# Kernel tuning notes

Measured on AMD Instinct MI355X. Metric: run time of the kernel, lower is better.

Reference implementation:

```python
import jax, jax.numpy as jnp
import numpy as np


def setup_inputs() -> dict:
    key = jax.random.key(0)
    ks = jax.random.split(key, 6)
    B_, S, D_in, D_out, R, E = 4, 2048, 2048, 2048, 64, 16
    x = jax.random.normal(ks[0], (B_, S, D_in), dtype=jnp.float32)
    W_base = jax.random.normal(ks[1], (D_out, D_in), dtype=jnp.float32) * (D_in ** -0.5)
    b_base = jax.random.normal(ks[2], (D_out,), dtype=jnp.float32) * 0.02
    # orthogonal rows, as get_orthogonal_matrix(reservoir_size, in_features)
    G = np.asarray(jax.random.normal(ks[3], (D_in, R), dtype=jnp.float32))
    Q, _ = np.linalg.qr(G)  # [D_in, R] orthonormal columns
    A = jnp.asarray(Q.T, dtype=jnp.float32)  # [R, D_in]
    # B initialized to zeros in the module; use small random so delta is nontrivial
    Bmat = jax.random.normal(ks[4], (E, D_out, R), dtype=jnp.float32) * 0.02
    W_router = jax.random.normal(ks[5], (E, D_in), dtype=jnp.float32) * 0.02
    return {"x": x, "W_base": W_base, "b_base": b_base, "A": A, "B": Bmat,
            "W_router": W_router, "top_k": 2}


def reference(x, W_base, b_base, A, B, W_router, top_k):
    E = W_router.shape[0]
    base_output = jnp.einsum('bsi,oi->bso', x, W_base) + b_base          # [B,S,D_out]
    res_hidden = jnp.einsum('bsi,ri->bsr', x, A)                          # [B,S,R]
    router_logits = jnp.einsum('bsi,ei->bse', x, W_router)                # [B,S,E]
    routing_weights = jax.nn.softmax(router_logits, axis=-1)
    if top_k > 0 and top_k < E:
        _, top_idx = jax.lax.top_k(routing_weights, top_k)                # [B,S,k]
        mask = jax.nn.one_hot(top_idx, E, dtype=routing_weights.dtype).sum(axis=-2)
        routing_weights = routing_weights * mask
        routing_weights = routing_weights / (routing_weights.sum(axis=-1, keepdims=True) + 1e-6)
    # contract experts+rank without materializing [B,S,E,D_out]
    h = jnp.einsum('bsr,bse->bser', res_hidden, routing_weights)          # [B,S,E,R] (small)
    delta = jnp.einsum('bser,edr->bsd', h, B)                             # [B,S,D_out]
    return base_output + delta
```

## Files before the change

### kernel.cpp

```cpp
#include <hip/hip_runtime.h>
#include <hip/hip_bf16.h>

#define D_IN  2048
#define D_OUT 2048
#define RNK   64
#define NE    16
#define KTOT  3072
#define NTILE 48

typedef __attribute__((ext_vector_type(8))) short bf16x8;
typedef __attribute__((ext_vector_type(4))) float f32x4;
typedef __attribute__((ext_vector_type(16))) float f32x16;

__device__ __forceinline__ void async_ld16(const void* g, void* l) {
    __builtin_amdgcn_global_load_lds(
        (const __attribute__((address_space(1))) void*)g,
        (__attribute__((address_space(3))) void*)l,
        16, 0, 0);
}

__global__ __launch_bounds__(384) void castwa_kernel(
    const float* __restrict__ Wb, const float* __restrict__ Bm,
    const float* __restrict__ A,
    __hip_bfloat16* __restrict__ Wc, __hip_bfloat16* __restrict__ Ab)
{
    const int c = threadIdx.x * 8;
    const float* src;
    __hip_bfloat16* dst;
    if (blockIdx.x < D_OUT) {
        const int n = blockIdx.x;
        if (c < D_IN) {
            src = Wb + (size_t)n * D_IN + c;
        } else {
            const int j = c - D_IN;
            const int e = j >> 6, r = j & 63;
            src = Bm + ((size_t)e * D_OUT + n) * RNK + r;
        }
        dst = Wc + (size_t)n * KTOT + c;
    } else {
        if (c >= D_IN) return;
        const int r = blockIdx.x - D_OUT;
        src = A + (size_t)r * D_IN + c;
        dst = Ab + (size_t)r * D_IN + c;
    }
    const float4 a = *(const float4*)src;
    const float4 b = *(const float4*)(src + 4);
    const float vv[8] = {a.x, a.y, a.z, a.w, b.x, b.y, b.z, b.w};
    union { bf16x8 v; __hip_bfloat16 h[8]; } u;
#pragma unroll
    for (int q = 0; q < 8; ++q) u.h[q] = __float2bfloat16(vv[q]);
    *(bf16x8*)dst = u.v;
}

__global__ __launch_bounds__(512) void prep2_kernel(
    const float* __restrict__ x, const float* __restrict__ Wr,
    const __hip_bfloat16* __restrict__ Ab,
    const int* __restrict__ topk_p, __hip_bfloat16* __restrict__ Xc)
{
    __shared__ __align__(16) char smem[81920];
    __hip_bfloat16* xb = (__hip_bfloat16*)smem;
    float* stage = (float*)(smem + 65536);
    float* red = (float*)smem;
    float* wf  = (float*)(smem + 65536);

    const int tid = threadIdx.x;
    const int wave = tid >> 6, lane = tid & 63;
    const int qm = lane & 15, quad = lane >> 4;
    const int t0 = blockIdx.x * 16;
    const int tA = t0 + wave * 2;

    float acc[NE][2];
#pragma unroll
    for (int e = 0; e < NE; ++e) { acc[e][0] = 0.f; acc[e][1] = 0.f; }

    const float4* x4 = (const float4*)x;
    float4 xv[2], xn[2];
    xv[0] = x4[(size_t)tA * 512 + lane];
    xv[1] = x4[(size_t)(tA + 1) * 512 + lane];

    for (int c = 0; c < 8; ++c) {
        async_ld16(Wr + (size_t)wave * D_IN + c * 256 + lane * 4,
                   (void*)(stage + wave * 256));
        async_ld16(Wr + (size_t)(wave + 8) * D_IN + c * 256 + lane * 4,
                   (void*)(stage + (wave + 8) * 256));
        if (c < 7) {
            xn[0] = x4[(size_t)tA * 512 + (c + 1) * 64 + lane];
            xn[1] = x4[(size_t)(tA + 1) * 512 + (c + 1) * 64 + lane];
        }
        __syncthreads();

#pragma unroll
        for (int t = 0; t < 2; ++t) {
            const int tl = wave * 2 + t;
            union { short4 v; __hip_bfloat16 h[4]; } u;
            u.h[0] = __float2bfloat16(xv[t].x); u.h[1] = __float2bfloat16(xv[t].y);
            u.h[2] = __float2bfloat16(xv[t].z); u.h[3] = __float2bfloat16(xv[t].w);
            *(short4*)(Xc + (size_t)(t0 + tl) * KTOT + c * 256 + lane * 4) = u.v;
            const int gg = c * 32 + (lane >> 1);
            const int pg = gg ^ (tl & 7);
            *(short4*)((char*)xb + tl * 4096 + pg * 16 + (lane & 1) * 8) = u.v;
        }
        const float4* wr4 = (const float4*)stage;
#pragma unroll
        for (int e = 0; e < NE; ++e) {
            const float4 wv = wr4[e * 64 + lane];
            acc[e][0] += xv[0].x*wv.x + xv[0].y*wv.y + xv[0].z*wv.z + xv[0].w*wv.w;
            acc[e][1] += xv[1].x*wv.x + xv[1].y*wv.y + xv[1].z*wv.z + xv[1].w*wv.w;
        }
        __syncthreads();
        if (c < 7) { xv[0] = xn[0]; xv[1] = xn[1]; }
    }

#pragma unroll
    for (int off = 32; off; off >>= 1)
#pragma unroll
        for (int e = 0; e < NE; ++e) {
            acc[e][0] += __shfl_xor(acc[e][0], off, 64);
            acc[e][1] += __shfl_xor(acc[e][1], off, 64);
        }
    if (lane < 2) {
        const int tt = lane;
        const int k = topk_p[0];
        float m = -1e30f;
#pragma unroll
        for (int e = 0; e < NE; ++e) m = fmaxf(m, acc[e][tt]);
        float w[NE]; float ssum = 0.f;
#pragma unroll
        for (int e = 0; e < NE; ++e) { w[e] = __expf(acc[e][tt] - m); ssum += w[e]; }
        const float inv = 1.f / ssum;
#pragma unroll
        for (int e = 0; e < NE; ++e) w[e] *= inv;
        float* wfout = wf + (size_t)(wave * 2 + tt) * NE;
        if (k > 0 && k < NE) {
            int chosen[NE];
#pragma unroll
            for (int e = 0; e < NE; ++e) chosen[e] = 0;
            float ksum = 0.f;
            for (int it = 0; it < k; ++it) {
                int bi = 0; float bv = -1.f;
                for (int e = 0; e < NE; ++e)
                    if (!chosen[e] && w[e] > bv) { bv = w[e]; bi = e; }
                chosen[bi] = 1; ksum += bv;
            }
            const float rinv = 1.f / (ksum + 1e-6f);
            for (int e = 0; e < NE; ++e) wfout[e] = chosen[e] ? w[e] * rinv : 0.f;
        } else {
            for (int e = 0; e < NE; ++e) wfout[e] = w[e];
        }
    }

    f32x4 racc[4] = {};
    const int kb = wave * 256;
#pragma unroll
    for (int s = 0; s < 4; ++s) {
        const int k0 = kb + s * 64;
        const int gg0 = (k0 >> 3) + quad;
        const bf16x8 a0 = *(const bf16x8*)((char*)xb + qm * 4096 + ((gg0 ^ (qm & 7)) * 16));
        const bf16x8 a1 = *(const bf16x8*)((char*)xb + qm * 4096 + (((gg0 + 4) ^ (qm & 7)) * 16));
        bf16x8 b0[4], b1[4];
#pragma unroll
        for (int nf = 0; nf < 4; ++nf) {
            const __hip_bfloat16* bp = Ab + (size_t)(qm + nf * 16) * D_IN + k0 + quad * 8;
            b0[nf] = *(const bf16x8*)bp;
            b1[nf] = *(const bf16x8*)(bp + 32);
        }
#pragma unroll
        for (int nf = 0; nf < 4; ++nf) {
            racc[nf] = __builtin_amdgcn_mfma_f32_16x16x32_bf16(a0, b0[nf], racc[nf], 0, 0, 0);
            racc[nf] = __builtin_amdgcn_mfma_f32_16x16x32_bf16(a1, b1[nf], racc[nf], 0, 0, 0);
        }
    }
    __syncthreads();

#pragma unroll
    for (int nf = 0; nf < 4; ++nf)
#pragma unroll
        for (int r = 0; r < 4; ++r)
            red[(wave * 16 + quad * 4 + r) * 64 + nf * 16 + qm] = racc[nf][r];
    __syncthreads();

#pragma unroll
    for (int it = 0; it < 4; ++it) {
        const int s = it * 512 + tid;
        const int t = s >> 7;
        const int chunk = s & 127;
        const int e = chunk >> 3, r0 = (chunk & 7) * 8;
        const float wgt = wf[t * 16 + e];
        float4 s0 = {0.f, 0.f, 0.f, 0.f}, s1 = {0.f, 0.f, 0.f, 0.f};
#pragma unroll
        for (int w2 = 0; w2 < 8; ++w2) {
            const float4 p0 = ((const float4*)red)[(w2 * 16 + t) * 16 + (r0 >> 2)];
            const float4 p1 = ((const float4*)red)[(w2 * 16 + t) * 16 + (r0 >> 2) + 1];
            s0.x += p0.x; s0.y += p0.y; s0.z += p0.z; s0.w += p0.w;
            s1.x += p1.x; s1.y += p1.y; s1.z += p1.z; s1.w += p1.w;
        }
        union { bf16x8 v; __hip_bfloat16 h[8]; } u;
        u.h[0] = __float2bfloat16(wgt * s0.x); u.h[1] = __float2bfloat16(wgt * s0.y);
        u.h[2] = __float2bfloat16(wgt * s0.z); u.h[3] = __float2bfloat16(wgt * s0.w);
        u.h[4] = __float2bfloat16(wgt * s1.x); u.h[5] = __float2bfloat16(wgt * s1.y);
        u.h[6] = __float2bfloat16(wgt * s1.z); u.h[7] = __float2bfloat16(wgt * s1.w);
        *(bf16x8*)(Xc + (size_t)(t0 + t) * KTOT + D_IN + chunk * 8) = u.v;
    }
}

#define LDA3(BUF, M, ks) (*(const bf16x8*)(smem + (BUF) + \
    ((((M) >> 1) * 128 + wm2 * 64 + ((M) & 1) * 32 + l31) * 128) + \
    (((((ks) * 2 + lhi) ^ (l31 & 7))) << 4)))
#define LDB3(BUF, N, ks) (*(const bf16x8*)(smem + 65536 + (BUF) + \
    ((wn4 * 64 + (N) * 32 + l31) * 128) + \
    (((((ks) * 2 + lhi) ^ (l31 & 7))) << 4)))

#define GP(BUF, MH, ISSUE, WAIT) do { \
    bf16x8 af[2][4]; \
    if ((MH) == 0) { \
        _Pragma("unroll") for (int n = 0; n < 2; ++n) \
        _Pragma("unroll") for (int ks = 0; ks < 4; ++ks) \
            bfr[n][ks] = LDB3(BUF, n, ks); \
    } \
    _Pragma("unroll") for (int m = 0; m < 2; ++m) \
    _Pragma("unroll") for (int ks = 0; ks < 4; ++ks) \
        af[m][ks] = LDA3(BUF, (MH) * 2 + m, ks); \
    ISSUE; \
    __builtin_amdgcn_s_setprio(1); \
    _Pragma("unroll") for (int ks = 0; ks < 4; ++ks) \
    _Pragma("unroll") for (int m = 0; m < 2; ++m) \
    _Pragma("unroll") for (int n = 0; n < 2; ++n) \
        acc[(MH) * 2 + m][n] = __builtin_amdgcn_mfma_f32_32x32x16_bf16( \
            af[m][ks], bfr[n][ks], acc[(MH) * 2 + m][n], 0, 0, 0); \
    __builtin_amdgcn_s_setprio(0); \
    WAIT; \
    __builtin_amdgcn_sched_barrier(0); \
    __builtin_amdgcn_s_barrier(); \
    __builtin_amdgcn_sched_barrier(0); \
} while (0)

__global__ __launch_bounds__(512, 2) void gemm3_kernel(
    const __hip_bfloat16* __restrict__ Am,
    const __hip_bfloat16* __restrict__ Bm,
    const float* __restrict__ bias,
    float* __restrict__ C)
{
    __shared__ __align__(16) char smem[131072];
    const int tid = threadIdx.x;
    const int w = tid >> 6, lane = tid & 63;
    const int l31 = lane & 31, lhi = lane >> 5;
    const int wm2 = w >> 2, wn4 = w & 3;

    int flat = blockIdx.y * gridDim.x + blockIdx.x;
    flat = (flat & 7) * 32 + (flat >> 3);
    const int bm = flat & 31, bn = flat >> 5;

    const int rb0 = w * 16 + (lane >> 3);
    const int rb1 = rb0 + 8;
    const int gs0 = (lane & 7) ^ (rb0 & 7);
    const int gs1 = (lane & 7) ^ (rb1 & 7);
    const __hip_bfloat16* pA0 = Am + (size_t)(bm * 256 + rb0) * KTOT + gs0 * 8;
    const __hip_bfloat16* pA1 = Am + (size_t)(bm * 256 + rb1) * KTOT + gs1 * 8;
    const __hip_bfloat16* pB0 = Bm + (size_t)(bn * 256 + rb0) * KTOT + gs0 * 8;
    const __hip_bfloat16* pB1 = Bm + (size_t)(bn * 256 + rb1) * KTOT + gs1 * 8;
    const size_t HO = (size_t)128 * KTOT;

    f32x16 acc[4][2] = {};
    bf16x8 bfr[2][4];

    auto stageP1 = [&](int tn) {
        const size_t ko = (size_t)tn * 64;
        char* da = smem + (tn & 1) * 32768 + w * 2048;
        async_ld16(pA0 + ko, da);
        async_ld16(pA1 + ko, da + 1024);
        char* db = smem + 65536 + (tn & 1) * 32768 + w * 2048;
        async_ld16(pB0 + ko, db);
        async_ld16(pB1 + ko, db + 1024);
        async_ld16(pB0 + HO + ko, db + 16384);
        async_ld16(pB1 + HO + ko, db + 16384 + 1024);
    };
    auto stageP2 = [&](int tn) {
        const size_t ko = (size_t)tn * 64;
        char* da = smem + (tn & 1) * 32768 + 16384 + w * 2048;
        async_ld16(pA0 + HO + ko, da);
        async_ld16(pA1 + HO + ko, da + 1024);
    };

    stageP1(0); stageP2(0); stageP1(1);
    asm volatile("s_waitcnt vmcnt(8)" ::: "memory");
    __builtin_amdgcn_sched_barrier(0);
    __builtin_amdgcn_s_barrier();
    __builtin_amdgcn_sched_barrier(0);

    for (int t = 0; t < NTILE - 2; ++t) {
        const int bo = (t & 1) * 32768;
        GP(bo, 0, stageP2(t + 1),
           asm volatile("s_waitcnt vmcnt(8)" ::: "memory"));
        GP(bo, 1, stageP1(t + 2),
           asm volatile("s_waitcnt vmcnt(8)" ::: "memory"));
    }
    {
        const int bo = ((NTILE - 2) & 1) * 32768;
        GP(bo, 0, stageP2(NTILE - 1),
           asm volatile("s_waitcnt vmcnt(8)" ::: "memory"));
        GP(bo, 1, ,
           asm volatile("s_waitcnt vmcnt(2)" ::: "memory"));
    }
    {
        const int bo = ((NTILE - 1) & 1) * 32768;
        GP(bo, 0, ,
           asm volatile("s_waitcnt vmcnt(0)" ::: "memory"));
        GP(bo, 1, , );
    }

#pragma unroll
    for (int n = 0; n < 2; ++n) {
        const int col = bn * 256 + wn4 * 64 + n * 32 + l31;
        const float bbv = bias[col];
#pragma unroll
        for (int m = 0; m < 4; ++m) {
            const size_t rbase = (size_t)bm * 256 + (m >> 1) * 128 + wm2 * 64
                               + (m & 1) * 32 + 4 * lhi;
#pragma unroll
            for (int reg = 0; reg < 16; ++reg) {
                const size_t row = rbase + (reg & 3) + 8 * (reg >> 2);
                C[row * D_OUT + col] = acc[m][n][reg] + bbv;
            }
        }
    }
}

extern "C" void kernel_launch(void* const* d_in, const int* in_sizes, int n_in,
                              void* d_out, int out_size, void* d_ws, size_t ws_size,
                              hipStream_t stream) {
    const float* x    = (const float*)d_in[0];
    const float* Wb   = (const float*)d_in[1];
    const float* bb   = (const float*)d_in[2];
    const float* A    = (const float*)d_in[3];
    const float* Bm   = (const float*)d_in[4];
    const float* Wr   = (const float*)d_in[5];
    const int*   topk = (const int*)d_in[6];
    float* out = (float*)d_out;
    const int T = in_sizes[0] / D_IN;

    __hip_bfloat16* Xc = (__hip_bfloat16*)d_ws;
    __hip_bfloat16* Wc = (__hip_bfloat16*)((char*)d_ws + (size_t)T * KTOT * 2);
    __hip_bfloat16* Ab = (__hip_bfloat16*)d_out;

    castwa_kernel<<<D_OUT + RNK, 384, 0, stream>>>(Wb, Bm, A, Wc, Ab);
    prep2_kernel<<<T / 16, 512, 0, stream>>>(x, Wr, Ab, topk, Xc);
    gemm3_kernel<<<dim3(32, 8), 512, 0, stream>>>(Xc, Wc, bb, out);
}
```

Measured before the change: 265.5 us.

## Double-buffer router weight staging in prep kernel and remap GEMM tiles per XCD

The prep kernel now gives each half-wave one token, processes 128-element chunks over 16 iterations, and double-buffers the router-weight staging in LDS. This replaces two __syncthreads per chunk with a single vmcnt wait plus barrier, so loads overlap with compute and the reduction needs fewer shuffle steps. The GEMM block-to-tile mapping is also changed so each XCD works on an 8x4 patch of output tiles, meant to improve L2 reuse of A and B panels. The costs are more loop iterations, a swizzled LDS layout, and an added barrier before the rank projection.

```diff
diff --git a/kernel.cpp b/kernel.cpp
--- a/kernel.cpp
+++ b/kernel.cpp
@@ -59,78 +59,73 @@
 {
     __shared__ __align__(16) char smem[81920];
     __hip_bfloat16* xb = (__hip_bfloat16*)smem;
-    float* stage = (float*)(smem + 65536);
+    float* stg = (float*)(smem + 65536);
     float* red = (float*)smem;
     float* wf  = (float*)(smem + 65536);
 
     const int tid = threadIdx.x;
     const int wave = tid >> 6, lane = tid & 63;
+    const int l31 = lane & 31, lh = lane >> 5;
     const int qm = lane & 15, quad = lane >> 4;
     const int t0 = blockIdx.x * 16;
-    const int tA = t0 + wave * 2;
-
-    float acc[NE][2];
-#pragma unroll
-    for (int e = 0; e < NE; ++e) { acc[e][0] = 0.f; acc[e][1] = 0.f; }
+    const int tl = wave * 2 + lh;
+    const size_t myt = (size_t)t0 + tl;
+
+    float acc[NE];
+#pragma unroll
+    for (int e = 0; e < NE; ++e) acc[e] = 0.f;
 
     const float4* x4 = (const float4*)x;
-    float4 xv[2], xn[2];
-    xv[0] = x4[(size_t)tA * 512 + lane];
-    xv[1] = x4[(size_t)(tA + 1) * 512 + lane];
-
-    for (int c = 0; c < 8; ++c) {
-        async_ld16(Wr + (size_t)wave * D_IN + c * 256 + lane * 4,
-                   (void*)(stage + wave * 256));
-        async_ld16(Wr + (size_t)(wave + 8) * D_IN + c * 256 + lane * 4,
-                   (void*)(stage + (wave + 8) * 256));
-        if (c < 7) {
-            xn[0] = x4[(size_t)tA * 512 + (c + 1) * 64 + lane];
-            xn[1] = x4[(size_t)(tA + 1) * 512 + (c + 1) * 64 + lane];
-        }
-        __syncthreads();
-
-#pragma unroll
-        for (int t = 0; t < 2; ++t) {
-            const int tl = wave * 2 + t;
-            union { short4 v; __hip_bfloat16 h[4]; } u;
-            u.h[0] = __float2bfloat16(xv[t].x); u.h[1] = __float2bfloat16(xv[t].y);
-            u.h[2] = __float2bfloat16(xv[t].z); u.h[3] = __float2bfloat16(xv[t].w);
-            *(short4*)(Xc + (size_t)(t0 + tl) * KTOT + c * 256 + lane * 4) = u.v;
-            const int gg = c * 32 + (lane >> 1);
-            const int pg = gg ^ (tl & 7);
-            *(short4*)((char*)xb + tl * 4096 + pg * 16 + (lane & 1) * 8) = u.v;
-        }
-        const float4* wr4 = (const float4*)stage;
+    const int sg = l31 ^ ((l31 >> 3) & 7);
+    const float* wr_src = Wr + (size_t)tl * D_IN + sg * 4;
+
+    async_ld16(wr_src, (void*)(stg + wave * 256));
+    float4 xv = x4[myt * 512 + l31];
+    float4 xn;
+
+    for (int c = 0; c < 16; ++c) {
+        asm volatile("s_waitcnt vmcnt(1)" ::: "memory");
+        __builtin_amdgcn_sched_barrier(0);
+        __builtin_amdgcn_s_barrier();
+        __builtin_amdgcn_sched_barrier(0);
+        if (c < 15) {
+            async_ld16(wr_src + (c + 1) * 128,
+                       (void*)(stg + ((c + 1) & 1) * 2048 + wave * 256));
+            xn = x4[myt * 512 + (c + 1) * 32 + l31];
+        }
+        union { short4 v; __hip_bfloat16 h[4]; } u;
+        u.h[0] = __float2bfloat16(xv.x); u.h[1] = __float2bfloat16(xv.y);
+        u.h[2] = __float2bfloat16(xv.z); u.h[3] = __float2bfloat16(xv.w);
+        *(short4*)(Xc + myt * KTOT + c * 128 + l31 * 4) = u.v;
+        const int G = c * 16 + (l31 >> 1);
+        *(short4*)((char*)xb + tl * 4096 + ((G ^ (tl & 7)) * 16)
+                   + (l31 & 1) * 8) = u.v;
+        const float* sb = stg + (c & 1) * 2048;
 #pragma unroll
         for (int e = 0; e < NE; ++e) {
-            const float4 wv = wr4[e * 64 + lane];
-            acc[e][0] += xv[0].x*wv.x + xv[0].y*wv.y + xv[0].z*wv.z + xv[0].w*wv.w;
-            acc[e][1] += xv[1].x*wv.x + xv[1].y*wv.y + xv[1].z*wv.z + xv[1].w*wv.w;
-        }
-        __syncthreads();
-        if (c < 7) { xv[0] = xn[0]; xv[1] = xn[1]; }
-    }
-
-#pragma unroll
-    for (int off = 32; off; off >>= 1)
-#pragma unroll
-        for (int e = 0; e < NE; ++e) {
-            acc[e][0] += __shfl_xor(acc[e][0], off, 64);
-            acc[e][1] += __shfl_xor(acc[e][1], off, 64);
-        }
-    if (lane < 2) {
-        const int tt = lane;
+            const float4 wv = *(const float4*)(sb + e * 128 + sg * 4);
+            acc[e] += xv.x * wv.x + xv.y * wv.y + xv.z * wv.z + xv.w * wv.w;
+        }
+        if (c < 15) xv = xn;
+    }
+
+#pragma unroll
+    for (int off = 16; off; off >>= 1)
+#pragma unroll
+        for (int e = 0; e < NE; ++e)
+            acc[e] += __shfl_xor(acc[e], off, 64);
+    if (l31 == 0) {
         const int k = topk_p[0];
         float m = -1e30f;
 #pragma unroll
-        for (int e = 0; e < NE; ++e) m = fmaxf(m, acc[e][tt]);
+        for (int e = 0; e < NE; ++e) m = fmaxf(m, acc[e]);
         float w[NE]; float ssum = 0.f;
 #pragma unroll
-        for (int e = 0; e < NE; ++e) { w[e] = __expf(acc[e][tt] - m); ssum += w[e]; }
+        for (int e = 0; e < NE; ++e) { w[e] = __expf(acc[e] - m); ssum += w[e]; }
         const float inv = 1.f / ssum;
 #pragma unroll
         for (int e = 0; e < NE; ++e) w[e] *= inv;
-        float* wfout = wf + (size_t)(wave * 2 + tt) * NE;
+        float* wfout = wf + (size_t)tl * NE;
         if (k > 0 && k < NE) {
             int chosen[NE];
 #pragma unroll
@@ -148,6 +143,7 @@
             for (int e = 0; e < NE; ++e) wfout[e] = w[e];
         }
     }
+    __syncthreads();
 
     f32x4 racc[4] = {};
     const int kb = wave * 256;
@@ -246,9 +242,10 @@
     const int l31 = lane & 31, lhi = lane >> 5;
     const int wm2 = w >> 2, wn4 = w & 3;
 
-    int flat = blockIdx.y * gridDim.x + blockIdx.x;
-    flat = (flat & 7) * 32 + (flat >> 3);
-    const int bm = flat & 31, bn = flat >> 5;
+    const int flat = blockIdx.y * gridDim.x + blockIdx.x;
+    const int xcd = flat & 7, j = flat >> 3;
+    const int bm = (xcd & 3) * 8 + (j & 7);
+    const int bn = (xcd >> 2) * 4 + (j >> 3);
 
     const int rb0 = w * 16 + (lane >> 3);
     const int rb1 = rb0 + 8;
```

New measurement: 263.4 us. About the same (-0.8%).
